# Kernel tuning notes

Hardware: AMD Instinct MI355X
Metric: run time of the kernel (lower is better)

## Reference

```python
import jax, jax.numpy as jnp
from jax import lax
import numpy as np

NUM_INPUTS = 512
NUM_HIDDENS = 1024
BATCH = 64
SEQ_LEN = 512


def setup_inputs() -> dict:
    key = jax.random.key(0)
    ks = jax.random.split(key, 8)
    D, H = NUM_INPUTS, NUM_HIDDENS
    w = lambda k, shape: 0.01 * jax.random.normal(k, shape, dtype=jnp.float32)
    return {
        "inputs": jax.random.normal(ks[0], (BATCH, SEQ_LEN, D), dtype=jnp.float32),
        "state": jax.random.normal(ks[1], (BATCH, H), dtype=jnp.float32),
        "W_xz": w(ks[2], (D, H)), "W_hz": w(ks[3], (H, H)), "b_z": jnp.zeros((H,), jnp.float32),
        "W_xr": w(ks[4], (D, H)), "W_hr": w(ks[5], (H, H)), "b_r": jnp.zeros((H,), jnp.float32),
        "W_xh": w(ks[6], (D, H)), "W_hh": w(ks[7], (H, H)), "b_h": jnp.zeros((H,), jnp.float32),
    }


def reference(inputs, state, W_xz, W_hz, b_z, W_xr, W_hr, b_r, W_xh, W_hh, b_h):
    B, T, _ = inputs.shape
    Hd = state.shape[1]
    # Precompute all input-side gate projections in three big GEMMs: [T, B, H]
    xz = (jnp.einsum('btd,dh->bth', inputs, W_xz) + b_z).transpose(1, 0, 2)
    xr = (jnp.einsum('btd,dh->bth', inputs, W_xr) + b_r).transpose(1, 0, 2)
    xh = (jnp.einsum('btd,dh->bth', inputs, W_xh) + b_h).transpose(1, 0, 2)

    def step(Hc, xs):
        xz_t, xr_t, xh_t = xs
        Z = jax.nn.sigmoid(xz_t + Hc @ W_hz)
        R = jax.nn.sigmoid(xr_t + Hc @ W_hr)
        H_tilda = jnp.tanh(xh_t + (R * Hc) @ W_hh)
        Hn = Z * Hc + (1.0 - Z) * H_tilda
        return Hn, Hn

    H_final, outs = lax.scan(step, state, (xz, xr, xh))  # outs: [T, B, H]
    # torch.cat(outputs, 0) -> [T*B, H]; .transpose(1, 0) -> [H, T*B]
    outputs = outs.reshape(T * B, Hd).T
    return outputs, H_final
```

## Files before the change

### kernel.cpp

```cpp
#include <hip/hip_runtime.h>
#include <hip/hip_bf16.h>

typedef unsigned short ushort_t;
typedef unsigned int uint32;
typedef unsigned long long ull;
typedef short bf16x8 __attribute__((ext_vector_type(8)));
typedef float f32x4 __attribute__((ext_vector_type(4)));

#define Bb 64
#define Tt 512
#define Dd 512
#define Hh 1024
#define KK 1536
#define NBLK 64
#define OUT2_OFF 33554432ull
#define FLAGS_OFF 9699328ull
#define XB_OFF    9707776ull
#define XB_BYTES  33554432ull


__device__ inline ushort_t f2b(float f) {
    __hip_bfloat16 h = __float2bfloat16(f);
    return __builtin_bit_cast(ushort_t, h);
}
__device__ inline float b2f(ushort_t u) {
    uint32 x = ((uint32)u) << 16;
    return __builtin_bit_cast(float, x);
}
__device__ inline bf16x8 ld_bf8(const ushort_t* p) {
    uint4 v = *reinterpret_cast<const uint4*>(p);
    return __builtin_bit_cast(bf16x8, v);
}
__device__ inline bf16x8 ld_x8(const float* p) {
    float4 u = *reinterpret_cast<const float4*>(p);
    float4 v = *reinterpret_cast<const float4*>(p + 4);
    bf16x8 a;
    a[0] = (short)f2b(u.x); a[1] = (short)f2b(u.y); a[2] = (short)f2b(u.z); a[3] = (short)f2b(u.w);
    a[4] = (short)f2b(v.x); a[5] = (short)f2b(v.y); a[6] = (short)f2b(v.z); a[7] = (short)f2b(v.w);
    return a;
}
__device__ inline uint4 ld_c16(const ushort_t* p) {
    uint4 d;
    asm volatile("global_load_dwordx4 %0, %1, off sc0 sc1" : "=v"(d) : "v"(p) : "memory");
    return d;
}
__device__ inline bf16x8 as_bf(uint4 v) { return __builtin_bit_cast(bf16x8, v); }
__device__ inline void st_a8(ushort_t* p, ull v) {
    __hip_atomic_store((ull*)p, v, __ATOMIC_RELAXED, __HIP_MEMORY_SCOPE_AGENT);
}
__device__ inline float sigm(float x) { return 1.f / (1.f + __expf(-x)); }

#define MFMA(a, b, c) __builtin_amdgcn_mfma_f32_16x16x32_bf16((a), (b), (c), 0, 0, 0)

__device__ inline void b_arrive(uint32* flags, uint32 val) {
    asm volatile("s_waitcnt vmcnt(0)" ::: "memory");
    __syncthreads();
    if (threadIdx.x == 0)
        __hip_atomic_store(flags + (uint32)blockIdx.x * 32, val,
                           __ATOMIC_RELAXED, __HIP_MEMORY_SCOPE_AGENT);
}
__device__ inline void b_wait(uint32* flags, uint32 val) {
    if (threadIdx.x < 64) {
        uint32 v;
        do {
            v = __hip_atomic_load(flags + threadIdx.x * 32,
                                  __ATOMIC_RELAXED, __HIP_MEMORY_SCOPE_AGENT);
        } while (__any((int)(v < val)));
    }
    __syncthreads();
    asm volatile("" ::: "memory");
}

__global__ __launch_bounds__(256) void k_init(const float* __restrict__ state,
                                              ushort_t* __restrict__ HB, uint32* flags) {
    int i = blockIdx.x * 256 + threadIdx.x;
    if (i < Bb * Hh) HB[i] = f2b(state[i]);
    if (i < 2112) flags[i] = 0;
}

__global__ __launch_bounds__(256) void k_xb(const float* __restrict__ inp,
                                            ushort_t* __restrict__ XB) {
    size_t i = ((size_t)blockIdx.x * 256 + threadIdx.x) * 8;
    bf16x8 v = ld_x8(inp + i);
    *reinterpret_cast<uint4*>(XB + i) = __builtin_bit_cast(uint4, v);
}

__global__ __launch_bounds__(256) void k_wt(const float* __restrict__ Wxz, const float* __restrict__ Whz,
                                            const float* __restrict__ Wxr, const float* __restrict__ Whr,
                                            const float* __restrict__ Wxh, const float* __restrict__ Whh,
                                            ushort_t* __restrict__ WT) {
    __shared__ float lds[64][65];
    int id = blockIdx.x;
    int g = id / 384, rem = id % 384, nt = rem / 24, kt = rem % 24;
    const float* Wx = (g == 0) ? Wxz : (g == 1) ? Wxr : Wxh;
    const float* Wh = (g == 0) ? Whz : (g == 1) ? Whr : Whh;
    int n0 = nt * 64, k0 = kt * 64;
    int tr = threadIdx.x >> 6, tc = threadIdx.x & 63;
    #pragma unroll
    for (int i = 0; i < 16; i++) {
        int kl = i * 4 + tr, k = k0 + kl;
        lds[kl][tc] = (k < 512) ? Wx[(size_t)k * Hh + n0 + tc]
                                : Wh[(size_t)(k - 512) * Hh + n0 + tc];
    }
    __syncthreads();
    #pragma unroll
    for (int i = 0; i < 16; i++) {
        int nl = i * 4 + tr;
        WT[((size_t)g * Hh + n0 + nl) * KK + k0 + tc] = f2b(lds[tc][nl]);
    }
}

__global__ __launch_bounds__(512, 2) void gru_persist(
    const float* __restrict__ inp, const ushort_t* __restrict__ XB, int use_xb,
    const float* __restrict__ bz, const float* __restrict__ br, const float* __restrict__ bh,
    ushort_t* HB, ushort_t* RH, const ushort_t* __restrict__ WT,
    uint32* flags, float* __restrict__ out) {
    __shared__ ushort_t WL[3 * 48 * 512];
    __shared__ float    XCH[4 * 256];
    __shared__ ushort_t STG[4 * 256];

    const int bi = blockIdx.x;
    const int tid = threadIdx.x;

    for (int idx = tid; idx < 9216; idx += 512) {
        int g = idx / 3072, r = idx % 3072, col = r / 192, c8 = r % 192;
        int kc = c8 >> 2, slot = c8 & 3, ps = slot ^ ((col >> 1) & 3);
        const ushort_t* src = WT + ((size_t)g * Hh + bi * 16 + col) * KK + c8 * 8;
        *reinterpret_cast<uint4*>(WL + g * 24576 + kc * 512 + col * 32 + ps * 8) =
            *reinterpret_cast<const uint4*>(src);
    }

    const int l = tid & 63, w = tid >> 6;
    const int m = w & 3;
    const bool isZ = (w < 4);
    const int lrow = l & 15, lq = l >> 4;
    const int ncol = bi * 16 + lrow;
    const int wloff = lrow * 32 + (lq ^ ((lrow >> 1) & 3)) * 8;

    #define WTILE(g, kc) ld_bf8(WL + (g) * 24576 + (kc) * 512 + wloff)

    const int arow = m * 16 + lrow;
    const float*    xF  = inp + (size_t)arow * (Tt * Dd) + lq * 8;
    const ushort_t* xBp = XB  + (size_t)arow * (Tt * Dd) + lq * 8;
    const ushort_t* hb  = HB  + arow * Hh + lq * 8;
    const ushort_t* rb  = RH  + arow * Hh + lq * 8 + (isZ ? 0 : 512);
    const int gA = isZ ? 0 : 1;
    const int kB = isZ ? 16 : 32;
    const float bzv = bz[ncol], brv = br[ncol], bhv = bh[ncol];
    const int xch_i = m * 256 + l * 4;

    const size_t strow  = (size_t)(w * 16 + (l >> 2)) * Hh + bi * 16 + (l & 3) * 4;
    const int    stg_wr = (w & 3) * 256;
    const int    stg_rd = (w & 3) * 256 + (l >> 2) * 16 + (l & 3) * 4;

    float hold[4];
    if (isZ) {
        #pragma unroll
        for (int j = 0; j < 4; j++)
            hold[j] = b2f(HB[(size_t)(m * 16 + lq * 4 + j) * Hh + ncol]);
    }

    __syncthreads();

    for (int t = 0; t < Tt; ++t) {
        bf16x8 xa[16];
        if (use_xb) {
            #pragma unroll
            for (int i = 0; i < 16; i++) xa[i] = ld_bf8(xBp + (size_t)t * Dd + i * 32);
        } else {
            #pragma unroll
            for (int i = 0; i < 16; i++) xa[i] = ld_x8(xF + (size_t)t * Dd + i * 32);
        }
        const f32x4 z4 = {0.f, 0.f, 0.f, 0.f};
        f32x4 g0 = z4, g1 = z4;
        if (isZ) {
            #pragma unroll
            for (int kk = 0; kk < 16; kk++) {
                g0 = MFMA(xa[kk], WTILE(0, kk), g0);
                g1 = MFMA(xa[kk], WTILE(2, kk), g1);
            }
        } else {
            #pragma unroll
            for (int kk = 0; kk < 16; kk++)
                g0 = MFMA(xa[kk], WTILE(1, kk), g0);
        }

        b_wait(flags, 2u * (uint32)t);

        uint4 Ah[32];
        #pragma unroll
        for (int i = 0; i < 32; i++) Ah[i] = ld_c16(hb + i * 32);
        asm volatile("s_waitcnt vmcnt(0)" ::: "memory");
        __builtin_amdgcn_sched_barrier(0);
        #pragma unroll
        for (int kk = 0; kk < 32; kk++)
            g0 = MFMA(as_bf(Ah[kk]), WTILE(gA, 16 + kk), g0);

        if (!isZ) {
            #pragma unroll
            for (int j = 0; j < 4; j++)
                XCH[m * 256 + (lq * 4 + j) * 16 + lrow] = sigm(g0[j] + brv);
        }
        __syncthreads();
        float zreg[4];
        if (isZ) {
            #pragma unroll
            for (int j = 0; j < 4; j++) {
                zreg[j] = sigm(g0[j] + bzv);
                float rr = XCH[m * 256 + (lq * 4 + j) * 16 + lrow];
                STG[stg_wr + (lq * 4 + j) * 16 + lrow] = f2b(rr * hold[j]);
            }
            asm volatile("s_waitcnt lgkmcnt(0)" ::: "memory");
            st_a8(RH + strow, *reinterpret_cast<const ull*>(&STG[stg_rd]));
        }
        b_arrive(flags, 2u * (uint32)t + 1u);
        b_wait(flags, 2u * (uint32)t + 1u);

        uint4 Ar[16];
        #pragma unroll
        for (int i = 0; i < 16; i++) Ar[i] = ld_c16(rb + i * 32);
        asm volatile("s_waitcnt vmcnt(0)" ::: "memory");
        __builtin_amdgcn_sched_barrier(0);
        f32x4 ha = z4, hbp = z4;
        #pragma unroll
        for (int kk = 0; kk < 16; kk += 2) {
            ha  = MFMA(as_bf(Ar[kk]),     WTILE(2, kB + kk),     ha);
            hbp = MFMA(as_bf(Ar[kk + 1]), WTILE(2, kB + kk + 1), hbp);
        }
        ha += hbp;
        if (!isZ) *reinterpret_cast<f32x4*>(&XCH[xch_i]) = ha;
        __syncthreads();
        if (isZ) {
            f32x4 tot = ha + g1 + *reinterpret_cast<const f32x4*>(&XCH[xch_i]);
            float hn[4];
            #pragma unroll
            for (int j = 0; j < 4; j++) {
                float pre = tot[j] + bhv;
                float e = __expf(-2.f * fabsf(pre));
                float th = (1.f - e) / (1.f + e);
                th = copysignf(th, pre);
                float v = zreg[j] * hold[j] + (1.f - zreg[j]) * th;
                hold[j] = v;
                hn[j] = v;
                STG[stg_wr + (lq * 4 + j) * 16 + lrow] = f2b(v);
            }
            asm volatile("s_waitcnt lgkmcnt(0)" ::: "memory");
            st_a8(HB + strow, *reinterpret_cast<const ull*>(&STG[stg_rd]));
            *reinterpret_cast<float4*>(out + (size_t)ncol * (Tt * Bb) + (size_t)t * Bb + m * 16 + lq * 4) =
                make_float4(hn[0], hn[1], hn[2], hn[3]);
            if (t == Tt - 1) {
                #pragma unroll
                for (int j = 0; j < 4; j++)
                    out[OUT2_OFF + (size_t)(m * 16 + lq * 4 + j) * Hh + ncol] = hn[j];
            }
        }
        b_arrive(flags, 2u * (uint32)t + 2u);
    }
    #undef WTILE
}

extern "C" void kernel_launch(void* const* d_in, const int* in_sizes, int n_in,
                              void* d_out, int out_size, void* d_ws, size_t ws_size,
                              hipStream_t stream) {
    const float* inp   = (const float*)d_in[0];
    const float* state = (const float*)d_in[1];
    const float* Wxz   = (const float*)d_in[2];
    const float* Whz   = (const float*)d_in[3];
    const float* bz    = (const float*)d_in[4];
    const float* Wxr   = (const float*)d_in[5];
    const float* Whr   = (const float*)d_in[6];
    const float* br    = (const float*)d_in[7];
    const float* Wxh   = (const float*)d_in[8];
    const float* Whh   = (const float*)d_in[9];
    const float* bh    = (const float*)d_in[10];
    float* out = (float*)d_out;

    char* ws = (char*)d_ws;
    ushort_t* HB    = (ushort_t*)(ws);
    ushort_t* RH    = (ushort_t*)(ws + 131072);
    ushort_t* WT    = (ushort_t*)(ws + 262144);
    uint32*   flags = (uint32*)(ws + FLAGS_OFF);
    ushort_t* XB    = (ushort_t*)(ws + XB_OFF);
    int use_xb = (ws_size >= XB_OFF + XB_BYTES) ? 1 : 0;

    k_init<<<dim3(256), dim3(256), 0, stream>>>(state, HB, flags);
    k_wt<<<dim3(1152), dim3(256), 0, stream>>>(Wxz, Whz, Wxr, Whr, Wxh, Whh, WT);
    if (use_xb)
        k_xb<<<dim3(8192), dim3(256), 0, stream>>>(inp, XB);

    void* args[] = {(void*)&inp, (void*)&XB, (void*)&use_xb,
                    (void*)&bz, (void*)&br, (void*)&bh,
                    (void*)&HB, (void*)&RH, (void*)&WT, (void*)&flags, (void*)&out};
    hipError_t e = hipLaunchCooperativeKernel((const void*)gru_persist, dim3(NBLK), dim3(512),
                                              args, 0, stream);
    if (e != hipSuccess) {
        gru_persist<<<dim3(NBLK), dim3(512), 0, stream>>>(inp, XB, use_xb, bz, br, bh,
                                                          HB, RH, WT, flags, out);
    }
}
```

Before: 9.906 ms.

## Use 256-thread blocks with chunked flag waits and prefetched input projections

Shrinks each persistent block from 8 waves to 4, each wave computing all three gates for its 16 batch rows, so the LDS exchange buffer and the intra-block gate split go away. The grid-wide barrier becomes a fine-grained wait: a fast path checks all flags at once, and otherwise each 256-column chunk of H or R*H is consumed as soon as its 16 producer blocks have arrived. The next step's input projection is loaded and computed after the current step's barrier work, taking it off the critical path. The cost is more MFMA work per wave with fewer waves to hide latency, plus extra flag polling traffic.

Result: faster. 8.898 ms (-10.2%).

```diff
diff --git a/kernel.cpp b/kernel.cpp
--- a/kernel.cpp
+++ b/kernel.cpp
@@ -48,28 +48,12 @@
 __device__ inline void st_a8(ushort_t* p, ull v) {
     __hip_atomic_store((ull*)p, v, __ATOMIC_RELAXED, __HIP_MEMORY_SCOPE_AGENT);
 }
+__device__ inline uint32 ld_flag(const uint32* p) {
+    return __hip_atomic_load(p, __ATOMIC_RELAXED, __HIP_MEMORY_SCOPE_AGENT);
+}
 __device__ inline float sigm(float x) { return 1.f / (1.f + __expf(-x)); }
 
 #define MFMA(a, b, c) __builtin_amdgcn_mfma_f32_16x16x32_bf16((a), (b), (c), 0, 0, 0)
-
-__device__ inline void b_arrive(uint32* flags, uint32 val) {
-    asm volatile("s_waitcnt vmcnt(0)" ::: "memory");
-    __syncthreads();
-    if (threadIdx.x == 0)
-        __hip_atomic_store(flags + (uint32)blockIdx.x * 32, val,
-                           __ATOMIC_RELAXED, __HIP_MEMORY_SCOPE_AGENT);
-}
-__device__ inline void b_wait(uint32* flags, uint32 val) {
-    if (threadIdx.x < 64) {
-        uint32 v;
-        do {
-            v = __hip_atomic_load(flags + threadIdx.x * 32,
-                                  __ATOMIC_RELAXED, __HIP_MEMORY_SCOPE_AGENT);
-        } while (__any((int)(v < val)));
-    }
-    __syncthreads();
-    asm volatile("" ::: "memory");
-}
 
 __global__ __launch_bounds__(256) void k_init(const float* __restrict__ state,
                                               ushort_t* __restrict__ HB, uint32* flags) {
@@ -110,19 +94,18 @@
     }
 }
 
-__global__ __launch_bounds__(512, 2) void gru_persist(
+__global__ __launch_bounds__(256, 1) void gru_persist(
     const float* __restrict__ inp, const ushort_t* __restrict__ XB, int use_xb,
     const float* __restrict__ bz, const float* __restrict__ br, const float* __restrict__ bh,
     ushort_t* HB, ushort_t* RH, const ushort_t* __restrict__ WT,
     uint32* flags, float* __restrict__ out) {
     __shared__ ushort_t WL[3 * 48 * 512];
-    __shared__ float    XCH[4 * 256];
     __shared__ ushort_t STG[4 * 256];
 
     const int bi = blockIdx.x;
     const int tid = threadIdx.x;
 
-    for (int idx = tid; idx < 9216; idx += 512) {
+    for (int idx = tid; idx < 9216; idx += 256) {
         int g = idx / 3072, r = idx % 3072, col = r / 192, c8 = r % 192;
         int kc = c8 >> 2, slot = c8 & 3, ps = slot ^ ((col >> 1) & 3);
         const ushort_t* src = WT + ((size_t)g * Hh + bi * 16 + col) * KK + c8 * 8;
@@ -131,130 +114,183 @@
     }
 
     const int l = tid & 63, w = tid >> 6;
-    const int m = w & 3;
-    const bool isZ = (w < 4);
     const int lrow = l & 15, lq = l >> 4;
     const int ncol = bi * 16 + lrow;
     const int wloff = lrow * 32 + (lq ^ ((lrow >> 1) & 3)) * 8;
+    const int c0 = bi & 3;
 
     #define WTILE(g, kc) ld_bf8(WL + (g) * 24576 + (kc) * 512 + wloff)
 
-    const int arow = m * 16 + lrow;
-    const float*    xF  = inp + (size_t)arow * (Tt * Dd) + lq * 8;
-    const ushort_t* xBp = XB  + (size_t)arow * (Tt * Dd) + lq * 8;
-    const ushort_t* hb  = HB  + arow * Hh + lq * 8;
-    const ushort_t* rb  = RH  + arow * Hh + lq * 8 + (isZ ? 0 : 512);
-    const int gA = isZ ? 0 : 1;
-    const int kB = isZ ? 16 : 32;
+    const int arow = w * 16 + lrow;
+    const float*    xF = inp + (size_t)arow * (Tt * Dd) + lq * 8;
+    const ushort_t* xBp = XB + (size_t)arow * (Tt * Dd) + lq * 8;
+    const ushort_t* hb = HB + arow * Hh + lq * 8;
+    const ushort_t* rb = RH + arow * Hh + lq * 8;
     const float bzv = bz[ncol], brv = br[ncol], bhv = bh[ncol];
-    const int xch_i = m * 256 + l * 4;
 
     const size_t strow  = (size_t)(w * 16 + (l >> 2)) * Hh + bi * 16 + (l & 3) * 4;
-    const int    stg_wr = (w & 3) * 256;
-    const int    stg_rd = (w & 3) * 256 + (l >> 2) * 16 + (l & 3) * 4;
+    const int    stg_wr = w * 256;
+    const int    stg_rd = w * 256 + (l >> 2) * 16 + (l & 3) * 4;
 
     float hold[4];
-    if (isZ) {
+    #pragma unroll
+    for (int j = 0; j < 4; j++)
+        hold[j] = b2f(HB[(size_t)(w * 16 + lq * 4 + j) * Hh + ncol]);
+
+    __syncthreads();
+
+    const f32x4 z4 = {0.f, 0.f, 0.f, 0.f};
+    f32x4 az = z4, ar = z4, ahx = z4;
+
+    bf16x8 xa[16];
+    if (use_xb) {
         #pragma unroll
-        for (int j = 0; j < 4; j++)
-            hold[j] = b2f(HB[(size_t)(m * 16 + lq * 4 + j) * Hh + ncol]);
-    }
-
-    __syncthreads();
+        for (int i = 0; i < 16; i++) xa[i] = ld_bf8(xBp + i * 32);
+    } else {
+        #pragma unroll
+        for (int i = 0; i < 16; i++) xa[i] = ld_x8(xF + i * 32);
+    }
+    #pragma unroll
+    for (int kk = 0; kk < 16; kk++) {
+        az  = MFMA(xa[kk], WTILE(0, kk), az);
+        ar  = MFMA(xa[kk], WTILE(1, kk), ar);
+        ahx = MFMA(xa[kk], WTILE(2, kk), ahx);
+    }
 
     for (int t = 0; t < Tt; ++t) {
-        bf16x8 xa[16];
-        if (use_xb) {
+        const uint32 valH = 2u * (uint32)t;
+        const uint32 valR = 2u * (uint32)t + 1u;
+
+        {
+            uint32 v = ld_flag(flags + l * 32);
+            if (__all((int)(v >= valH))) {
+                uint4 A[32];
+                #pragma unroll
+                for (int i = 0; i < 32; i++) A[i] = ld_c16(hb + i * 32);
+                asm volatile("s_waitcnt vmcnt(0)" ::: "memory");
+                __builtin_amdgcn_sched_barrier(0);
+                #pragma unroll
+                for (int kk = 0; kk < 32; kk++) {
+                    az = MFMA(as_bf(A[kk]), WTILE(0, 16 + kk), az);
+                    ar = MFMA(as_bf(A[kk]), WTILE(1, 16 + kk), ar);
+                }
+            } else {
+                for (int ci = 0; ci < 4; ci++) {
+                    int c = (c0 + ci) & 3;
+                    uint32 vv;
+                    do { vv = ld_flag(flags + (c * 16 + (l & 15)) * 32); }
+                    while (__any((int)(vv < valH)));
+                    uint4 A[8];
+                    #pragma unroll
+                    for (int i = 0; i < 8; i++) A[i] = ld_c16(hb + (c * 8 + i) * 32);
+                    asm volatile("s_waitcnt vmcnt(0)" ::: "memory");
+                    __builtin_amdgcn_sched_barrier(0);
+                    #pragma unroll
+                    for (int i = 0; i < 8; i++) {
+                        int kk = c * 8 + i;
+                        az = MFMA(as_bf(A[i]), WTILE(0, 16 + kk), az);
+                        ar = MFMA(as_bf(A[i]), WTILE(1, 16 + kk), ar);
+                    }
+                }
+            }
+        }
+        float zreg[4];
+        #pragma unroll
+        for (int j = 0; j < 4; j++) {
+            zreg[j] = sigm(az[j] + bzv);
+            float rr = sigm(ar[j] + brv);
+            STG[stg_wr + (lq * 4 + j) * 16 + lrow] = f2b(rr * hold[j]);
+        }
+        asm volatile("s_waitcnt lgkmcnt(0)" ::: "memory");
+        st_a8(RH + strow, *reinterpret_cast<const ull*>(&STG[stg_rd]));
+        asm volatile("s_waitcnt vmcnt(0)" ::: "memory");
+        __syncthreads();
+        if (tid == 0)
+            __hip_atomic_store(flags + (uint32)bi * 32, valR,
+                               __ATOMIC_RELAXED, __HIP_MEMORY_SCOPE_AGENT);
+
+        if (t < Tt - 1) {
+            if (use_xb) {
+                #pragma unroll
+                for (int i = 0; i < 16; i++) xa[i] = ld_bf8(xBp + (size_t)(t + 1) * Dd + i * 32);
+            } else {
+                #pragma unroll
+                for (int i = 0; i < 16; i++) xa[i] = ld_x8(xF + (size_t)(t + 1) * Dd + i * 32);
+            }
+        }
+
+        f32x4 ah0 = ahx, ah1 = z4;
+        {
+            uint32 v = ld_flag(flags + l * 32);
+            if (__all((int)(v >= valR))) {
+                uint4 A[32];
+                #pragma unroll
+                for (int i = 0; i < 32; i++) A[i] = ld_c16(rb + i * 32);
+                asm volatile("s_waitcnt vmcnt(0)" ::: "memory");
+                __builtin_amdgcn_sched_barrier(0);
+                #pragma unroll
+                for (int kk = 0; kk < 32; kk += 2) {
+                    ah0 = MFMA(as_bf(A[kk]),     WTILE(2, 16 + kk),     ah0);
+                    ah1 = MFMA(as_bf(A[kk + 1]), WTILE(2, 16 + kk + 1), ah1);
+                }
+            } else {
+                for (int ci = 0; ci < 4; ci++) {
+                    int c = (c0 + ci) & 3;
+                    uint32 vv;
+                    do { vv = ld_flag(flags + (c * 16 + (l & 15)) * 32); }
+                    while (__any((int)(vv < valR)));
+                    uint4 A[8];
+                    #pragma unroll
+                    for (int i = 0; i < 8; i++) A[i] = ld_c16(rb + (c * 8 + i) * 32);
+                    asm volatile("s_waitcnt vmcnt(0)" ::: "memory");
+                    __builtin_amdgcn_sched_barrier(0);
+                    #pragma unroll
+                    for (int i = 0; i < 8; i++) {
+                        int kk = c * 8 + i;
+                        if (i & 1) ah1 = MFMA(as_bf(A[i]), WTILE(2, 16 + kk), ah1);
+                        else       ah0 = MFMA(as_bf(A[i]), WTILE(2, 16 + kk), ah0);
+                    }
+                }
+            }
+        }
+        f32x4 aht = ah0 + ah1;
+        float hn[4];
+        #pragma unroll
+        for (int j = 0; j < 4; j++) {
+            float pre = aht[j] + bhv;
+            float e = __expf(-2.f * fabsf(pre));
+            float th = (1.f - e) / (1.f + e);
+            th = copysignf(th, pre);
+            float v = zreg[j] * hold[j] + (1.f - zreg[j]) * th;
+            hold[j] = v;
+            hn[j] = v;
+            STG[stg_wr + (lq * 4 + j) * 16 + lrow] = f2b(v);
+        }
+        asm volatile("s_waitcnt lgkmcnt(0)" ::: "memory");
+        st_a8(HB + strow, *reinterpret_cast<const ull*>(&STG[stg_rd]));
+        asm volatile("s_waitcnt vmcnt(0)" ::: "memory");
+        __syncthreads();
+        if (tid == 0)
+            __hip_atomic_store(flags + (uint32)bi * 32, valR + 1u,
+                               __ATOMIC_RELAXED, __HIP_MEMORY_SCOPE_AGENT);
+
+        *reinterpret_cast<float4*>(out + (size_t)ncol * (Tt * Bb) + (size_t)t * Bb + w * 16 + lq * 4) =
+            make_float4(hn[0], hn[1], hn[2], hn[3]);
+        if (t == Tt - 1) {
             #pragma unroll
-            for (int i = 0; i < 16; i++) xa[i] = ld_bf8(xBp + (size_t)t * Dd + i * 32);
-        } else {
-            #pragma unroll
-            for (int i = 0; i < 16; i++) xa[i] = ld_x8(xF + (size_t)t * Dd + i * 32);
-        }
-        const f32x4 z4 = {0.f, 0.f, 0.f, 0.f};
-        f32x4 g0 = z4, g1 = z4;
-        if (isZ) {
+            for (int j = 0; j < 4; j++)
+                out[OUT2_OFF + (size_t)(w * 16 + lq * 4 + j) * Hh + ncol] = hn[j];
+        }
+
+        az = z4; ar = z4; ahx = z4;
+        if (t < Tt - 1) {
             #pragma unroll
             for (int kk = 0; kk < 16; kk++) {
-                g0 = MFMA(xa[kk], WTILE(0, kk), g0);
-                g1 = MFMA(xa[kk], WTILE(2, kk), g1);
+                az  = MFMA(xa[kk], WTILE(0, kk), az);
+                ar  = MFMA(xa[kk], WTILE(1, kk), ar);
+                ahx = MFMA(xa[kk], WTILE(2, kk), ahx);
             }
-        } else {
-            #pragma unroll
-            for (int kk = 0; kk < 16; kk++)
-                g0 = MFMA(xa[kk], WTILE(1, kk), g0);
-        }
-
-        b_wait(flags, 2u * (uint32)t);
-
-        uint4 Ah[32];
-        #pragma unroll
-        for (int i = 0; i < 32; i++) Ah[i] = ld_c16(hb + i * 32);
-        asm volatile("s_waitcnt vmcnt(0)" ::: "memory");
-        __builtin_amdgcn_sched_barrier(0);
-        #pragma unroll
-        for (int kk = 0; kk < 32; kk++)
-            g0 = MFMA(as_bf(Ah[kk]), WTILE(gA, 16 + kk), g0);
-
-        if (!isZ) {
-            #pragma unroll
-            for (int j = 0; j < 4; j++)
-                XCH[m * 256 + (lq * 4 + j) * 16 + lrow] = sigm(g0[j] + brv);
-        }
-        __syncthreads();
-        float zreg[4];
-        if (isZ) {
-            #pragma unroll
-            for (int j = 0; j < 4; j++) {
-                zreg[j] = sigm(g0[j] + bzv);
-                float rr = XCH[m * 256 + (lq * 4 + j) * 16 + lrow];
-                STG[stg_wr + (lq * 4 + j) * 16 + lrow] = f2b(rr * hold[j]);
-            }
-            asm volatile("s_waitcnt lgkmcnt(0)" ::: "memory");
-            st_a8(RH + strow, *reinterpret_cast<const ull*>(&STG[stg_rd]));
-        }
-        b_arrive(flags, 2u * (uint32)t + 1u);
-        b_wait(flags, 2u * (uint32)t + 1u);
-
-        uint4 Ar[16];
-        #pragma unroll
-        for (int i = 0; i < 16; i++) Ar[i] = ld_c16(rb + i * 32);
-        asm volatile("s_waitcnt vmcnt(0)" ::: "memory");
-        __builtin_amdgcn_sched_barrier(0);
-        f32x4 ha = z4, hbp = z4;
-        #pragma unroll
-        for (int kk = 0; kk < 16; kk += 2) {
-            ha  = MFMA(as_bf(Ar[kk]),     WTILE(2, kB + kk),     ha);
-            hbp = MFMA(as_bf(Ar[kk + 1]), WTILE(2, kB + kk + 1), hbp);
-        }
-        ha += hbp;
-        if (!isZ) *reinterpret_cast<f32x4*>(&XCH[xch_i]) = ha;
-        __syncthreads();
-        if (isZ) {
-            f32x4 tot = ha + g1 + *reinterpret_cast<const f32x4*>(&XCH[xch_i]);
-            float hn[4];
-            #pragma unroll
-            for (int j = 0; j < 4; j++) {
-                float pre = tot[j] + bhv;
-                float e = __expf(-2.f * fabsf(pre));
-                float th = (1.f - e) / (1.f + e);
-                th = copysignf(th, pre);
-                float v = zreg[j] * hold[j] + (1.f - zreg[j]) * th;
-                hold[j] = v;
-                hn[j] = v;
-                STG[stg_wr + (lq * 4 + j) * 16 + lrow] = f2b(v);
-            }
-            asm volatile("s_waitcnt lgkmcnt(0)" ::: "memory");
-            st_a8(HB + strow, *reinterpret_cast<const ull*>(&STG[stg_rd]));
-            *reinterpret_cast<float4*>(out + (size_t)ncol * (Tt * Bb) + (size_t)t * Bb + m * 16 + lq * 4) =
-                make_float4(hn[0], hn[1], hn[2], hn[3]);
-            if (t == Tt - 1) {
-                #pragma unroll
-                for (int j = 0; j < 4; j++)
-                    out[OUT2_OFF + (size_t)(m * 16 + lq * 4 + j) * Hh + ncol] = hn[j];
-            }
-        }
-        b_arrive(flags, 2u * (uint32)t + 2u);
+        }
     }
     #undef WTILE
 }
@@ -291,10 +327,10 @@
     void* args[] = {(void*)&inp, (void*)&XB, (void*)&use_xb,
                     (void*)&bz, (void*)&br, (void*)&bh,
                     (void*)&HB, (void*)&RH, (void*)&WT, (void*)&flags, (void*)&out};
-    hipError_t e = hipLaunchCooperativeKernel((const void*)gru_persist, dim3(NBLK), dim3(512),
+    hipError_t e = hipLaunchCooperativeKernel((const void*)gru_persist, dim3(NBLK), dim3(256),
                                               args, 0, stream);
     if (e != hipSuccess) {
-        gru_persist<<<dim3(NBLK), dim3(512), 0, stream>>>(inp, XB, use_xb, bz, br, bh,
+        gru_persist<<<dim3(NBLK), dim3(256), 0, stream>>>(inp, XB, use_xb, bz, br, bh,
                                                           HB, RH, WT, flags, out);
     }
 }
```
